# Optimization experiments

Hardware: AMD Instinct MI355X
Metric: run time of the kernel (lower is better)

Reference implementation:

```python
import jax, jax.numpy as jnp
import numpy as np

N = 8192

def setup_inputs() -> dict:
    key = jax.random.key(0)
    adj = jax.random.uniform(key, (N, N), dtype=jnp.float32)  # nonnegative weights
    return {"adj": adj}

def reference(adj) -> jnp.ndarray:
    # Symmetrize: adj + adj_T*(adj_T>adj) - adj*(adj_T>adj) == elementwise max(adj, adj^T)
    a = jnp.maximum(adj, adj.T)
    # Add self-loops: set diagonal to exactly 1 (adj + diag(1 - diag_part(adj)))
    n = a.shape[0]
    eye = jnp.eye(n, dtype=jnp.bool_)
    a = jnp.where(eye, jnp.ones((), a.dtype), a)
    # D^{-1/2} A D^{-1/2}: diag matmuls are equivalent to row/col scaling (O(n^2))
    d_inv_sqrt = jax.lax.rsqrt(jnp.sum(a, axis=1))  # [N]
    return a * d_inv_sqrt[:, None] * d_inv_sqrt[None, :]
```

## Files before the change

kernel.cpp:

```cpp
#include <hip/hip_runtime.h>

#define N 8192
#define T 64
#define TILES (N / T)
#define NPAIRS (TILES * (TILES + 1) / 2)
#define LDS_STRIDE 65
#define BLOCK 512

__device__ inline void decode_pair(int p, int& bi, int& bj) {
    float t = (float)TILES + 0.5f;
    int g = (int)(t - sqrtf(t * t - 2.0f * (float)p));
    if (g < 0) g = 0;
    if (g > TILES - 1) g = TILES - 1;
    while (g < TILES - 1 && ((g + 1) * TILES - (g + 1) * g / 2) <= p) g++;
    while (g > 0 && (g * TILES - g * (g - 1) / 2) > p) g--;
    bi = g;
    bj = bi + (p - (bi * TILES - bi * (bi - 1) / 2));
}

__device__ inline void load_tile(const float* __restrict__ src, int row0, int col0,
                                 float* lds) {
    int t = threadIdx.x;
    int c4 = t & 15;
    int r0 = t >> 4;
    #pragma unroll
    for (int rr = r0; rr < T; rr += 32) {
        const float4 v = *(const float4*)(src + (size_t)(row0 + rr) * N + col0 + c4 * 4);
        float* d = lds + rr * LDS_STRIDE + c4 * 4;
        d[0] = v.x; d[1] = v.y; d[2] = v.z; d[3] = v.w;
    }
}

__global__ __launch_bounds__(BLOCK) void k_rowsum(const float* __restrict__ adj,
                                                  float* __restrict__ rowsum) {
    __shared__ float ldsA[T * LDS_STRIDE];
    __shared__ float ldsB[T * LDS_STRIDE];
    __shared__ float red[BLOCK];
    int bi, bj;
    decode_pair((int)blockIdx.x, bi, bj);

    load_tile(adj, bi * T, bj * T, ldsA);
    load_tile(adj, bj * T, bi * T, ldsB);
    __syncthreads();

    int t = threadIdx.x;
    int lane = t & 63;
    int w = t >> 6;

    float acc = 0.0f;
    #pragma unroll
    for (int k = 0; k < 8; k++) {
        int c = w * 8 + k;
        float m = fmaxf(ldsA[lane * LDS_STRIDE + c], ldsB[c * LDS_STRIDE + lane]);
        if (bi == bj && lane == c) m = 1.0f;
        acc += m;
    }
    red[t] = acc;
    __syncthreads();
    if (t < 64) {
        float s = 0.0f;
        #pragma unroll
        for (int w2 = 0; w2 < 8; w2++) s += red[w2 * 64 + t];
        atomicAdd(&rowsum[bi * T + t], s);
    }

    if (bi != bj) {
        __syncthreads();
        float acc2 = 0.0f;
        #pragma unroll
        for (int k = 0; k < 8; k++) {
            int r = w * 8 + k;
            acc2 += fmaxf(ldsA[r * LDS_STRIDE + lane], ldsB[lane * LDS_STRIDE + r]);
        }
        red[t] = acc2;
        __syncthreads();
        if (t < 64) {
            float s = 0.0f;
            #pragma unroll
            for (int w2 = 0; w2 < 8; w2++) s += red[w2 * 64 + t];
            atomicAdd(&rowsum[bj * T + t], s);
        }
    }
}

__global__ __launch_bounds__(BLOCK) void k_scale(const float* __restrict__ adj,
                                                 const float* __restrict__ rowsum,
                                                 float* __restrict__ out) {
    __shared__ float ldsA[T * LDS_STRIDE];
    __shared__ float ldsB[T * LDS_STRIDE];
    __shared__ float dinvA[T];
    __shared__ float dinvB[T];
    int bi, bj;
    decode_pair((int)blockIdx.x, bi, bj);

    int t = threadIdx.x;
    if (t < 64)       dinvA[t]      = rsqrtf(rowsum[bi * T + t]);
    else if (t < 128) dinvB[t - 64] = rsqrtf(rowsum[bj * T + (t - 64)]);
    load_tile(adj, bi * T, bj * T, ldsA);
    load_tile(adj, bj * T, bi * T, ldsB);
    __syncthreads();

    int c4 = t & 15;
    int r0 = t >> 4;
    #pragma unroll
    for (int rr = r0; rr < T; rr += 32) {
        float4 v;
        float* vp = &v.x;
        #pragma unroll
        for (int k = 0; k < 4; k++) {
            int cc = c4 * 4 + k;
            float m = fmaxf(ldsA[rr * LDS_STRIDE + cc], ldsB[cc * LDS_STRIDE + rr]);
            if (bi == bj && rr == cc) m = 1.0f;
            vp[k] = m * dinvA[rr] * dinvB[cc];
        }
        *(float4*)(out + (size_t)(bi * T + rr) * N + bj * T + c4 * 4) = v;
    }
    if (bi != bj) {
        #pragma unroll
        for (int rr = r0; rr < T; rr += 32) {
            float4 v;
            float* vp = &v.x;
            #pragma unroll
            for (int k = 0; k < 4; k++) {
                int cc = c4 * 4 + k;
                float m = fmaxf(ldsB[rr * LDS_STRIDE + cc], ldsA[cc * LDS_STRIDE + rr]);
                vp[k] = m * dinvB[rr] * dinvA[cc];
            }
            *(float4*)(out + (size_t)(bj * T + rr) * N + bi * T + c4 * 4) = v;
        }
    }
}

extern "C" void kernel_launch(void* const* d_in, const int* in_sizes, int n_in,
                              void* d_out, int out_size, void* d_ws, size_t ws_size,
                              hipStream_t stream) {
    const float* adj = (const float*)d_in[0];
    float* out = (float*)d_out;
    float* rowsum = (float*)d_ws;

    hipMemsetAsync(rowsum, 0, N * sizeof(float), stream);
    k_rowsum<<<NPAIRS, BLOCK, 0, stream>>>(adj, rowsum);
    k_scale<<<NPAIRS, BLOCK, 0, stream>>>(adj, rowsum, out);
}
```

Measured before the change: 499.8 us.

## Use persistent 128x128 tile-pair kernels with register prefetch and swizzled LDS

Both kernels become persistent grids of 512 blocks of 1024 threads, each looping over 128x128 tile pairs. The next pair's global loads are issued into registers while the current pair is processed, so memory latency overlaps compute. An XOR-swizzled LDS layout replaces padding to keep transposed reads free of bank conflicts. Diagonal tiles load only one tile, the row and column sums are computed in a single pass, and output uses nontemporal stores. The larger tiles raise LDS use to 128KB per block, which can limit occupancy, and the serial pair-decode loop adds per-iteration cost.

```diff
diff --git a/kernel.cpp b/kernel.cpp
--- a/kernel.cpp
+++ b/kernel.cpp
@@ -1,133 +1,201 @@
 #include <hip/hip_runtime.h>
 
 #define N 8192
-#define T 64
-#define TILES (N / T)
-#define NPAIRS (TILES * (TILES + 1) / 2)
-#define LDS_STRIDE 65
-#define BLOCK 512
+#define TT 128
+#define TILES (N / TT)
+#define NP (TILES * (TILES + 1) / 2)
+#define GRID 512
+#define BLOCK 1024
+#define SWZ(r) ((r) & 31)
+
+typedef float nfloat4 __attribute__((ext_vector_type(4)));
+
+__device__ inline void lds_barrier() {
+    asm volatile("s_waitcnt lgkmcnt(0)" ::: "memory");
+    __builtin_amdgcn_s_barrier();
+}
 
 __device__ inline void decode_pair(int p, int& bi, int& bj) {
-    float t = (float)TILES + 0.5f;
-    int g = (int)(t - sqrtf(t * t - 2.0f * (float)p));
-    if (g < 0) g = 0;
-    if (g > TILES - 1) g = TILES - 1;
-    while (g < TILES - 1 && ((g + 1) * TILES - (g + 1) * g / 2) <= p) g++;
-    while (g > 0 && (g * TILES - g * (g - 1) / 2) > p) g--;
-    bi = g;
-    bj = bi + (p - (bi * TILES - bi * (bi - 1) / 2));
-}
-
-__device__ inline void load_tile(const float* __restrict__ src, int row0, int col0,
-                                 float* lds) {
-    int t = threadIdx.x;
-    int c4 = t & 15;
-    int r0 = t >> 4;
+    int g = 0, rem = p;
+    #pragma unroll 1
+    while (rem >= TILES - g) { rem -= TILES - g; g++; }
+    bi = g; bj = g + rem;
+}
+
+__device__ inline void issue_loads(const float* __restrict__ adj, int bi, int bj,
+                                   bool diag, int t, float4 va[4], float4 vb[4]) {
     #pragma unroll
-    for (int rr = r0; rr < T; rr += 32) {
-        const float4 v = *(const float4*)(src + (size_t)(row0 + rr) * N + col0 + c4 * 4);
-        float* d = lds + rr * LDS_STRIDE + c4 * 4;
-        d[0] = v.x; d[1] = v.y; d[2] = v.z; d[3] = v.w;
+    for (int k = 0; k < 4; k++) {
+        int f = k * BLOCK + t;
+        int row = f >> 5, j = f & 31;
+        va[k] = *(const float4*)(adj + (size_t)(bi * TT + row) * N + bj * TT + j * 4);
+    }
+    if (!diag) {
+        #pragma unroll
+        for (int k = 0; k < 4; k++) {
+            int f = k * BLOCK + t;
+            int row = f >> 5, j = f & 31;
+            vb[k] = *(const float4*)(adj + (size_t)(bj * TT + row) * N + bi * TT + j * 4);
+        }
+    }
+}
+
+__device__ inline void write_stage(int t, const float4 va[4], const float4 vb[4],
+                                   float* ldsA, float* ldsB, bool diag) {
+    #pragma unroll
+    for (int k = 0; k < 4; k++) {
+        int f = k * BLOCK + t;
+        int row = f >> 5, j = f & 31;
+        int off = row * TT + ((j ^ SWZ(row)) << 2);
+        *(float4*)(ldsA + off) = va[k];
+        if (!diag) *(float4*)(ldsB + off) = vb[k];
     }
 }
 
 __global__ __launch_bounds__(BLOCK) void k_rowsum(const float* __restrict__ adj,
                                                   float* __restrict__ rowsum) {
-    __shared__ float ldsA[T * LDS_STRIDE];
-    __shared__ float ldsB[T * LDS_STRIDE];
+    __shared__ float ldsA[TT * TT];
+    __shared__ float ldsB[TT * TT];
     __shared__ float red[BLOCK];
-    int bi, bj;
-    decode_pair((int)blockIdx.x, bi, bj);
-
-    load_tile(adj, bi * T, bj * T, ldsA);
-    load_tile(adj, bj * T, bi * T, ldsB);
-    __syncthreads();
-
     int t = threadIdx.x;
-    int lane = t & 63;
-    int w = t >> 6;
-
-    float acc = 0.0f;
-    #pragma unroll
-    for (int k = 0; k < 8; k++) {
-        int c = w * 8 + k;
-        float m = fmaxf(ldsA[lane * LDS_STRIDE + c], ldsB[c * LDS_STRIDE + lane]);
-        if (bi == bj && lane == c) m = 1.0f;
-        acc += m;
-    }
-    red[t] = acc;
-    __syncthreads();
-    if (t < 64) {
-        float s = 0.0f;
+    int r = t & 127;
+    int q = t >> 7;
+
+    int p = (int)blockIdx.x;
+    int bi, bj; decode_pair(p, bi, bj);
+    bool diag = (bi == bj);
+    float4 va[4], vb[4];
+    issue_loads(adj, bi, bj, diag, t, va, vb);
+
+    for (;;) {
+        write_stage(t, va, vb, ldsA, ldsB, diag);
+        int pn = p + GRID;
+        bool more = (pn < NP);
+        int nbi = 0, nbj = 0; bool ndiag = false;
+        if (more) {
+            decode_pair(pn, nbi, nbj);
+            ndiag = (nbi == nbj);
+            issue_loads(adj, nbi, nbj, ndiag, t, va, vb);
+        }
+        lds_barrier();
+
+        const float* LB = diag ? ldsA : ldsB;
+        float rowAcc = 0.f, colAcc = 0.f;
         #pragma unroll
-        for (int w2 = 0; w2 < 8; w2++) s += red[w2 * 64 + t];
-        atomicAdd(&rowsum[bi * T + t], s);
-    }
-
-    if (bi != bj) {
-        __syncthreads();
-        float acc2 = 0.0f;
-        #pragma unroll
-        for (int k = 0; k < 8; k++) {
-            int r = w * 8 + k;
-            acc2 += fmaxf(ldsA[r * LDS_STRIDE + lane], ldsB[lane * LDS_STRIDE + r]);
-        }
-        red[t] = acc2;
-        __syncthreads();
-        if (t < 64) {
-            float s = 0.0f;
+        for (int kk = 0; kk < 4; kk++) {
+            int j = q * 4 + kk;
+            int roff = r * TT + ((j ^ SWZ(r)) << 2);
+            float4 a4 = *(const float4*)(ldsA + roff);
+            float4 b4 = diag ? a4 : *(const float4*)(ldsB + roff);
             #pragma unroll
-            for (int w2 = 0; w2 < 8; w2++) s += red[w2 * 64 + t];
-            atomicAdd(&rowsum[bj * T + t], s);
-        }
+            for (int x = 0; x < 4; x++) {
+                int c = j * 4 + x;
+                int tof = c * TT + (((r >> 2) ^ SWZ(c)) << 2) + (r & 3);
+                float a_cr = ldsA[tof];
+                float b_cr = LB[tof];
+                float m1 = fmaxf(((const float*)&a4)[x], b_cr);
+                if (diag && r == c) m1 = 1.0f;
+                rowAcc += m1;
+                if (!diag)
+                    colAcc += fmaxf(((const float*)&b4)[x], a_cr);
+            }
+        }
+        lds_barrier();
+
+        red[t] = rowAcc;
+        lds_barrier();
+        if (t < 128) {
+            float s = 0.f;
+            #pragma unroll
+            for (int qq = 0; qq < 8; qq++) s += red[qq * 128 + t];
+            atomicAdd(&rowsum[bi * TT + t], s);
+        }
+        if (!diag) {
+            lds_barrier();
+            red[t] = colAcc;
+            lds_barrier();
+            if (t < 128) {
+                float s = 0.f;
+                #pragma unroll
+                for (int qq = 0; qq < 8; qq++) s += red[qq * 128 + t];
+                atomicAdd(&rowsum[bj * TT + t], s);
+            }
+        }
+        if (!more) break;
+        p = pn; bi = nbi; bj = nbj; diag = ndiag;
     }
 }
 
 __global__ __launch_bounds__(BLOCK) void k_scale(const float* __restrict__ adj,
                                                  const float* __restrict__ rowsum,
                                                  float* __restrict__ out) {
-    __shared__ float ldsA[T * LDS_STRIDE];
-    __shared__ float ldsB[T * LDS_STRIDE];
-    __shared__ float dinvA[T];
-    __shared__ float dinvB[T];
-    int bi, bj;
-    decode_pair((int)blockIdx.x, bi, bj);
-
+    __shared__ float ldsA[TT * TT];
+    __shared__ float ldsB[TT * TT];
+    __shared__ float dA[TT];
+    __shared__ float dB[TT];
     int t = threadIdx.x;
-    if (t < 64)       dinvA[t]      = rsqrtf(rowsum[bi * T + t]);
-    else if (t < 128) dinvB[t - 64] = rsqrtf(rowsum[bj * T + (t - 64)]);
-    load_tile(adj, bi * T, bj * T, ldsA);
-    load_tile(adj, bj * T, bi * T, ldsB);
-    __syncthreads();
-
-    int c4 = t & 15;
-    int r0 = t >> 4;
-    #pragma unroll
-    for (int rr = r0; rr < T; rr += 32) {
-        float4 v;
-        float* vp = &v.x;
+
+    int p = (int)blockIdx.x;
+    int bi, bj; decode_pair(p, bi, bj);
+    bool diag = (bi == bj);
+    float4 va[4], vb[4];
+    float rsv = 0.f;
+    issue_loads(adj, bi, bj, diag, t, va, vb);
+    if (t < 128)      rsv = rowsum[bi * TT + t];
+    else if (t < 256) rsv = rowsum[bj * TT + (t - 128)];
+
+    for (;;) {
+        write_stage(t, va, vb, ldsA, ldsB, diag);
+        if (t < 128)      dA[t]       = rsqrtf(rsv);
+        else if (t < 256) dB[t - 128] = rsqrtf(rsv);
+        int pn = p + GRID;
+        bool more = (pn < NP);
+        int nbi = 0, nbj = 0; bool ndiag = false;
+        if (more) {
+            decode_pair(pn, nbi, nbj);
+            ndiag = (nbi == nbj);
+            issue_loads(adj, nbi, nbj, ndiag, t, va, vb);
+            if (t < 128)      rsv = rowsum[nbi * TT + t];
+            else if (t < 256) rsv = rowsum[nbj * TT + (t - 128)];
+        }
+        lds_barrier();
+
+        const float* LB = diag ? ldsA : ldsB;
         #pragma unroll
         for (int k = 0; k < 4; k++) {
-            int cc = c4 * 4 + k;
-            float m = fmaxf(ldsA[rr * LDS_STRIDE + cc], ldsB[cc * LDS_STRIDE + rr]);
-            if (bi == bj && rr == cc) m = 1.0f;
-            vp[k] = m * dinvA[rr] * dinvB[cc];
-        }
-        *(float4*)(out + (size_t)(bi * T + rr) * N + bj * T + c4 * 4) = v;
-    }
-    if (bi != bj) {
-        #pragma unroll
-        for (int rr = r0; rr < T; rr += 32) {
-            float4 v;
-            float* vp = &v.x;
+            int f = k * BLOCK + t;
+            int row = f >> 5, j = f & 31;
+            int roff = row * TT + ((j ^ SWZ(row)) << 2);
+            float4 a4 = *(const float4*)(ldsA + roff);
+            nfloat4 v;
             #pragma unroll
-            for (int k = 0; k < 4; k++) {
-                int cc = c4 * 4 + k;
-                float m = fmaxf(ldsB[rr * LDS_STRIDE + cc], ldsA[cc * LDS_STRIDE + rr]);
-                vp[k] = m * dinvB[rr] * dinvA[cc];
-            }
-            *(float4*)(out + (size_t)(bj * T + rr) * N + bi * T + c4 * 4) = v;
-        }
+            for (int x = 0; x < 4; x++) {
+                int c = j * 4 + x;
+                int tof = c * TT + (((row >> 2) ^ SWZ(c)) << 2) + (row & 3);
+                float m = fmaxf(((const float*)&a4)[x], LB[tof]);
+                if (diag && row == c) m = 1.0f;
+                v[x] = m * dA[row] * dB[c];
+            }
+            __builtin_nontemporal_store(v,
+                (nfloat4*)(out + (size_t)(bi * TT + row) * N + bj * TT + j * 4));
+            if (!diag) {
+                float4 b4 = *(const float4*)(ldsB + roff);
+                nfloat4 u;
+                #pragma unroll
+                for (int x = 0; x < 4; x++) {
+                    int c = j * 4 + x;
+                    int tof = c * TT + (((row >> 2) ^ SWZ(c)) << 2) + (row & 3);
+                    float m = fmaxf(((const float*)&b4)[x], ldsA[tof]);
+                    u[x] = m * dB[row] * dA[c];
+                }
+                __builtin_nontemporal_store(u,
+                    (nfloat4*)(out + (size_t)(bj * TT + row) * N + bi * TT + j * 4));
+            }
+        }
+        lds_barrier();
+
+        if (!more) break;
+        p = pn; bi = nbi; bj = nbj; diag = ndiag;
     }
 }
 
@@ -138,7 +206,7 @@
     float* out = (float*)d_out;
     float* rowsum = (float*)d_ws;
 
-    hipMemsetAsync(rowsum, 0, N * sizeof(float), stream);
-    k_rowsum<<<NPAIRS, BLOCK, 0, stream>>>(adj, rowsum);
-    k_scale<<<NPAIRS, BLOCK, 0, stream>>>(adj, rowsum, out);
-}
+    (void)hipMemsetAsync(rowsum, 0, N * sizeof(float), stream);
+    k_rowsum<<<GRID, BLOCK, 0, stream>>>(adj, rowsum);
+    k_scale<<<GRID, BLOCK, 0, stream>>>(adj, rowsum, out);
+}
```

After: 667.1 us. +33.5%, slower.
